# Kernel optimization log

Measured on AMD Instinct MI355X. Metric: run time of the kernel, lower is better.

Reference implementation:

```python
import jax, jax.numpy as jnp
import numpy as np

B, S, D, E, K = 4, 2048, 768, 8, 2


def setup_inputs() -> dict:
    key = jax.random.key(0)
    ks = jax.random.split(key, 5)
    s = 0.02
    return {
        "x": jax.random.normal(ks[0], (B, S, D), dtype=jnp.float32),
        "gate_w": jax.random.normal(ks[1], (D, E), dtype=jnp.float32) * s,
        "gate_b": jnp.zeros((E,), dtype=jnp.float32),
        "w1": jax.random.normal(ks[2], (E, D, D), dtype=jnp.float32) * s,
        "b1": jnp.zeros((E, D), dtype=jnp.float32),
        "w2": jax.random.normal(ks[3], (E, D, D), dtype=jnp.float32) * s,
        "b2": jnp.zeros((E, D), dtype=jnp.float32),
    }


def reference(x, gate_w, gate_b, w1, b1, w2, b2):
    # MoE forward, eval mode (no gate noise, dropout = identity)
    b, s, d = x.shape
    xf = x.reshape(-1, d)                                  # [T, D]
    T = xf.shape[0]

    gate_logits = xf @ gate_w + gate_b                     # [T, E]
    gate_scores = jax.nn.softmax(gate_logits, axis=-1)

    topv, topi = jax.lax.top_k(gate_scores, K)             # [T, K]
    topv = topv / (jnp.sum(topv, axis=-1, keepdims=True) + 1e-8)

    # scatter top-k weights into dense per-expert combine weights [T, E]
    comb = jnp.zeros((T, E), dtype=xf.dtype).at[
        jnp.arange(T)[:, None], topi].add(topv)

    # expert MLPs (dense over experts; combine weights zero-out unselected)
    h = jax.nn.relu(jnp.einsum('td,edh->teh', xf, w1) + b1)  # [T, E, D]
    y = jnp.einsum('teh,eho->teo', h, w2) + b2               # [T, E, D]
    out = jnp.einsum('te,teo->to', comb, y).reshape(b, s, -1)

    # load-balance aux loss (CV^2 of expert importance)
    importance = gate_scores.sum(axis=0)                   # [E]
    cv2 = importance.var() / (importance.mean() ** 2 + 1e-8)
    aux_loss = 0.01 * cv2
    return out, aux_loss
```

## Files before the change

kernel.cpp:

```cpp
#include <hip/hip_runtime.h>


#define T_TOK 8192
#define D_DIM 768
#define E_EXP 8
#define TK    16384

typedef __attribute__((ext_vector_type(4))) float f32x4;
typedef __attribute__((ext_vector_type(8))) short s16x8;
typedef __attribute__((ext_vector_type(8))) unsigned short u16x8;

static __device__ __forceinline__ unsigned short f2bf(float f) {
    union { float f; unsigned u; } v; v.f = f;
    unsigned r = v.u + 0x7FFFu + ((v.u >> 16) & 1u);
    return (unsigned short)(r >> 16);
}
static __device__ __forceinline__ float bf2f(unsigned short h) {
    union { unsigned u; float f; } v; v.u = ((unsigned)h) << 16;
    return v.f;
}

__global__ __launch_bounds__(256) void gate_kernel(
    const float* __restrict__ x, const float* __restrict__ gw,
    const float* __restrict__ gb, unsigned short* __restrict__ xb,
    int* __restrict__ ea, int* __restrict__ eb,
    float* __restrict__ wa, float* __restrict__ wb,
    int* __restrict__ counts, float* __restrict__ importance)
{
    __shared__ float s_imp[4][8];
    __shared__ int   s_cnt[4][8];
    const int tid = threadIdx.x, wid = tid >> 6, lane = tid & 63;
    const int wg = blockIdx.x * 4 + wid;

    float imp[8]; int cnt[8];
    #pragma unroll
    for (int e = 0; e < 8; ++e) { imp[e] = 0.f; cnt[e] = 0; }

    for (int i = 0; i < 8; ++i) {
        const int t = wg + i * 1024;
        const float* xr = x + (size_t)t * D_DIM;
        float xv[12];
        float acc[8];
        #pragma unroll
        for (int e = 0; e < 8; ++e) acc[e] = 0.f;
        #pragma unroll
        for (int j = 0; j < 12; ++j) {
            const int d = lane + j * 64;
            float v = xr[d];
            xv[j] = v;
            xb[(size_t)t * D_DIM + d] = f2bf(v);
        }
        #pragma unroll
        for (int j = 0; j < 12; ++j) {
            const int d = lane + j * 64;
            const f32x4* g = (const f32x4*)(gw + (size_t)d * 8);
            f32x4 g0 = g[0], g1 = g[1];
            float v = xv[j];
            acc[0] += v * g0[0]; acc[1] += v * g0[1];
            acc[2] += v * g0[2]; acc[3] += v * g0[3];
            acc[4] += v * g1[0]; acc[5] += v * g1[1];
            acc[6] += v * g1[2]; acc[7] += v * g1[3];
        }
        #pragma unroll
        for (int s = 1; s < 64; s <<= 1) {
            #pragma unroll
            for (int e = 0; e < 8; ++e) acc[e] += __shfl_xor(acc[e], s);
        }
        float lg[8], mx = -1e30f;
        #pragma unroll
        for (int e = 0; e < 8; ++e) { lg[e] = acc[e] + gb[e]; mx = fmaxf(mx, lg[e]); }
        float p[8], ssum = 0.f;
        #pragma unroll
        for (int e = 0; e < 8; ++e) { p[e] = expf(lg[e] - mx); ssum += p[e]; }
        float sc[8];
        float inv_s = 1.f / ssum;
        #pragma unroll
        for (int e = 0; e < 8; ++e) { sc[e] = p[e] * inv_s; imp[e] += sc[e]; }
        int i0 = 0;
        #pragma unroll
        for (int e = 1; e < 8; ++e) if (sc[e] > sc[i0]) i0 = e;
        int i1 = (i0 == 0) ? 1 : 0;
        #pragma unroll
        for (int e = 0; e < 8; ++e) if (e != i0 && sc[e] > sc[i1]) i1 = e;
        float v0 = sc[i0], v1 = sc[i1];
        float inv = 1.f / (v0 + v1 + 1e-8f);
        if (lane == 0) {
            ea[t] = i0; eb[t] = i1; wa[t] = v0 * inv; wb[t] = v1 * inv;
            cnt[i0]++; cnt[i1]++;
        }
    }
    if (lane == 0) {
        #pragma unroll
        for (int e = 0; e < 8; ++e) { s_imp[wid][e] = imp[e]; s_cnt[wid][e] = cnt[e]; }
    }
    __syncthreads();
    if (tid < 8) {
        float si = 0.f; int sc2 = 0;
        #pragma unroll
        for (int w = 0; w < 4; ++w) { si += s_imp[w][tid]; sc2 += s_cnt[w][tid]; }
        atomicAdd(importance + tid, si);
        atomicAdd(counts + tid, sc2);
    }
}

__global__ void prefix_aux_kernel(const int* __restrict__ counts, int* __restrict__ basep,
                                  int* __restrict__ cursor,
                                  const float* __restrict__ importance,
                                  float* __restrict__ aux_out)
{
    if (threadIdx.x == 0 && blockIdx.x == 0) {
        int b = 0;
        for (int e = 0; e < 8; ++e) { basep[e] = b; cursor[e] = b; b += counts[e]; }
        float mean = 0.f;
        for (int e = 0; e < 8; ++e) mean += importance[e];
        mean *= 0.125f;
        float var = 0.f;
        for (int e = 0; e < 8; ++e) { float d = importance[e] - mean; var += d * d; }
        var *= 0.125f;
        aux_out[0] = 0.01f * var / (mean * mean + 1e-8f);
    }
}

__global__ __launch_bounds__(256) void scatter_kernel(
    const int* __restrict__ ea, const int* __restrict__ eb,
    const float* __restrict__ wa, const float* __restrict__ wb,
    int* __restrict__ cursor, int* __restrict__ list,
    float* __restrict__ wgt, int* __restrict__ slot)
{
    const int t = blockIdx.x * 256 + threadIdx.x;
    const int lane = threadIdx.x & 63;
    #pragma unroll
    for (int k = 0; k < 2; ++k) {
        const int e = k ? eb[t] : ea[t];
        const float w = k ? wb[t] : wa[t];
        int pos = 0;
        for (int ex = 0; ex < 8; ++ex) {
            unsigned long long m = __ballot(e == ex);
            if (e == ex) {
                int leader = __ffsll((unsigned long long)m) - 1;
                int n = __popcll(m);
                int p0 = 0;
                if (lane == leader) p0 = atomicAdd(cursor + ex, n);
                p0 = __shfl(p0, leader);
                pos = p0 + __popcll(m & ((1ull << lane) - 1ull));
            }
        }
        list[pos] = t; wgt[pos] = w; slot[t * 2 + k] = pos;
    }
}

__global__ __launch_bounds__(256) void tconv_kernel(
    const float* __restrict__ w1, const float* __restrict__ w2,
    unsigned short* __restrict__ w1t, unsigned short* __restrict__ w2t)
{
    const int z = blockIdx.z;
    const float* src = (z < 8 ? w1 : w2) + (size_t)(z & 7) * D_DIM * D_DIM;
    unsigned short* dst = (z < 8 ? w1t : w2t) + (size_t)(z & 7) * D_DIM * D_DIM;
    __shared__ float tile[32][33];
    const int tx = threadIdx.x, ty = threadIdx.y;
    const int k0 = blockIdx.x * 32, n0 = blockIdx.y * 32;
    #pragma unroll
    for (int j = 0; j < 4; ++j)
        tile[ty + j * 8][tx] = src[(size_t)(k0 + ty + j * 8) * D_DIM + n0 + tx];
    __syncthreads();
    #pragma unroll
    for (int j = 0; j < 4; ++j)
        dst[(size_t)(n0 + ty + j * 8) * D_DIM + k0 + tx] = f2bf(tile[tx][ty + j * 8]);
}

template<int GATHER, int RELU>
__global__ __launch_bounds__(256) void moe_gemm_kernel(
    const unsigned short* __restrict__ A, const unsigned short* __restrict__ Bt,
    const float* __restrict__ bias, unsigned short* __restrict__ C,
    const int* __restrict__ counts, const int* __restrict__ basep,
    const int* __restrict__ list)
{
    const int e = blockIdx.z;
    const int count = counts[e];
    const int m0 = blockIdx.x * 128;
    if (m0 >= count) return;
    const int n0 = blockIdx.y * 128;
    const int base = basep[e];

    __shared__ unsigned short Al[128][40];
    __shared__ unsigned short Bl[128][40];

    const int tid = threadIdx.x;
    const int lane = tid & 63, wid = tid >> 6;
    const int wr = wid >> 1, wc = wid & 1;

    const int srow = tid >> 2;
    const int scol = (tid & 3) * 8;

    long ga0, ga1;
    {
        int r0 = m0 + srow;      r0 = r0 < count ? r0 : count - 1;
        int r1 = m0 + 64 + srow; r1 = r1 < count ? r1 : count - 1;
        long gr0, gr1;
        if (GATHER) { gr0 = list[base + r0]; gr1 = list[base + r1]; }
        else        { gr0 = base + r0;       gr1 = base + r1; }
        ga0 = gr0 * D_DIM; ga1 = gr1 * D_DIM;
    }
    const long gb0 = ((long)e * D_DIM + n0 + srow) * D_DIM;
    const long gb1 = ((long)e * D_DIM + n0 + 64 + srow) * D_DIM;

    f32x4 acc[4][4];
    #pragma unroll
    for (int mi = 0; mi < 4; ++mi)
        #pragma unroll
        for (int ni = 0; ni < 4; ++ni)
            acc[mi][ni] = (f32x4)(0.f);

    for (int k0 = 0; k0 < D_DIM; k0 += 32) {
        u16x8 a0  = *(const u16x8*)(A  + ga0 + k0 + scol);
        u16x8 a1  = *(const u16x8*)(A  + ga1 + k0 + scol);
        u16x8 b0  = *(const u16x8*)(Bt + gb0 + k0 + scol);
        u16x8 b1v = *(const u16x8*)(Bt + gb1 + k0 + scol);
        __syncthreads();
        *(u16x8*)&Al[srow][scol]      = a0;
        *(u16x8*)&Al[64 + srow][scol] = a1;
        *(u16x8*)&Bl[srow][scol]      = b0;
        *(u16x8*)&Bl[64 + srow][scol] = b1v;
        __syncthreads();

        s16x8 af[4], bf[4];
        #pragma unroll
        for (int mi = 0; mi < 4; ++mi)
            af[mi] = *(const s16x8*)&Al[wr * 64 + mi * 16 + (lane & 15)][(lane >> 4) * 8];
        #pragma unroll
        for (int ni = 0; ni < 4; ++ni)
            bf[ni] = *(const s16x8*)&Bl[wc * 64 + ni * 16 + (lane & 15)][(lane >> 4) * 8];
        #pragma unroll
        for (int mi = 0; mi < 4; ++mi)
            #pragma unroll
            for (int ni = 0; ni < 4; ++ni)
                acc[mi][ni] = __builtin_amdgcn_mfma_f32_16x16x32_bf16(
                    af[mi], bf[ni], acc[mi][ni], 0, 0, 0);
    }

    #pragma unroll
    for (int ni = 0; ni < 4; ++ni) {
        const int cn = n0 + wc * 64 + ni * 16 + (lane & 15);
        const float bv = bias[e * D_DIM + cn];
        #pragma unroll
        for (int mi = 0; mi < 4; ++mi) {
            #pragma unroll
            for (int j = 0; j < 4; ++j) {
                const int rm = m0 + wr * 64 + mi * 16 + (lane >> 4) * 4 + j;
                if (rm < count) {
                    float v = acc[mi][ni][j] + bv;
                    if (RELU) v = fmaxf(v, 0.f);
                    C[(size_t)(base + rm) * D_DIM + cn] = f2bf(v);
                }
            }
        }
    }
}

__global__ __launch_bounds__(256) void combine_kernel(
    const unsigned short* __restrict__ y, const int* __restrict__ slot,
    const float* __restrict__ wgt, float* __restrict__ out)
{
    const int g = blockIdx.x * 256 + threadIdx.x;
    const int t = g / 96;
    const int n = (g % 96) * 8;
    const int s0 = slot[t * 2], s1 = slot[t * 2 + 1];
    const float w0 = wgt[s0], w1 = wgt[s1];
    u16x8 ya = *(const u16x8*)(y + (size_t)s0 * D_DIM + n);
    u16x8 yb = *(const u16x8*)(y + (size_t)s1 * D_DIM + n);
    f32x4 o0, o1;
    #pragma unroll
    for (int i = 0; i < 4; ++i) o0[i] = w0 * bf2f(ya[i])     + w1 * bf2f(yb[i]);
    #pragma unroll
    for (int i = 0; i < 4; ++i) o1[i] = w0 * bf2f(ya[4 + i]) + w1 * bf2f(yb[4 + i]);
    float* op = out + (size_t)t * D_DIM + n;
    *(f32x4*)op       = o0;
    *(f32x4*)(op + 4) = o1;
}

extern "C" void kernel_launch(void* const* d_in, const int* in_sizes, int n_in,
                              void* d_out, int out_size, void* d_ws, size_t ws_size,
                              hipStream_t stream)
{
    const float* x  = (const float*)d_in[0];
    const float* gw = (const float*)d_in[1];
    const float* gb = (const float*)d_in[2];
    const float* w1 = (const float*)d_in[3];
    const float* b1 = (const float*)d_in[4];
    const float* w2 = (const float*)d_in[5];
    const float* b2 = (const float*)d_in[6];
    float* out = (float*)d_out;

    char* ws = (char*)d_ws;
    size_t off = 0;
    auto alloc = [&](size_t bytes) {
        char* p = ws + off; off += (bytes + 255) & ~(size_t)255; return p;
    };
    unsigned short* xb  = (unsigned short*)alloc((size_t)T_TOK * D_DIM * 2);
    unsigned short* w1t = (unsigned short*)alloc((size_t)E_EXP * D_DIM * D_DIM * 2);
    unsigned short* w2t = (unsigned short*)alloc((size_t)E_EXP * D_DIM * D_DIM * 2);
    unsigned short* h   = (unsigned short*)alloc((size_t)TK * D_DIM * 2);
    unsigned short* y   = (unsigned short*)alloc((size_t)TK * D_DIM * 2);
    int*   list = (int*)alloc(TK * 4);
    float* wgt  = (float*)alloc(TK * 4);
    int*   slot = (int*)alloc(TK * 4);
    int*   ea   = (int*)alloc(T_TOK * 4);
    int*   eb   = (int*)alloc(T_TOK * 4);
    float* wa   = (float*)alloc(T_TOK * 4);
    float* wb   = (float*)alloc(T_TOK * 4);
    int*   meta = (int*)alloc(256);
    int*   counts = meta;
    int*   basep  = meta + 8;
    int*   cursor = meta + 16;
    float* importance = (float*)(meta + 24);

    hipMemsetAsync(meta, 0, 256, stream);
    tconv_kernel<<<dim3(24, 24, 16), dim3(32, 8), 0, stream>>>(w1, w2, w1t, w2t);
    gate_kernel<<<256, 256, 0, stream>>>(x, gw, gb, xb, ea, eb, wa, wb, counts, importance);
    prefix_aux_kernel<<<1, 64, 0, stream>>>(counts, basep, cursor, importance,
                                            out + (out_size - 1));
    scatter_kernel<<<32, 256, 0, stream>>>(ea, eb, wa, wb, cursor, list, wgt, slot);
    moe_gemm_kernel<1, 1><<<dim3(64, 6, 8), 256, 0, stream>>>(xb, w1t, b1, h, counts, basep, list);
    moe_gemm_kernel<0, 0><<<dim3(64, 6, 8), 256, 0, stream>>>(h, w2t, b2, y, counts, basep, list);
    combine_kernel<<<3072, 256, 0, stream>>>(y, slot, wgt, out);
}
```

Measured before the change: 338.1 us.

## Load GEMM tiles directly to LDS and fold prefix/aux into gate kernel

The expert GEMM now uses global_load_lds to move A and B tiles from global memory straight into shared memory, skipping the register round trip. The LDS tiles switch to an unpadded 32-element row stride that this instruction needs. Separately, the prefix-sum and aux-loss kernel is merged into the gate kernel through a last-block-done atomic counter, which removes one launch. Dropping the padding can cause LDS bank conflicts on the fragment reads, and loads are still not double-buffered.

```diff
diff --git a/kernel.cpp b/kernel.cpp
--- a/kernel.cpp
+++ b/kernel.cpp
@@ -18,6 +18,13 @@
 static __device__ __forceinline__ float bf2f(unsigned short h) {
     union { unsigned u; float f; } v; v.u = ((unsigned)h) << 16;
     return v.f;
+}
+
+static __device__ __forceinline__ void gload_lds16(const unsigned short* g, unsigned short* l) {
+    __builtin_amdgcn_global_load_lds(
+        (const __attribute__((address_space(1))) unsigned int*)(const void*)g,
+        (__attribute__((address_space(3))) unsigned int*)(void*)l,
+        16, 0, 0);
 }
 
 __global__ __launch_bounds__(256) void gate_kernel(
@@ -25,7 +32,9 @@
     const float* __restrict__ gb, unsigned short* __restrict__ xb,
     int* __restrict__ ea, int* __restrict__ eb,
     float* __restrict__ wa, float* __restrict__ wb,
-    int* __restrict__ counts, float* __restrict__ importance)
+    int* __restrict__ counts, float* __restrict__ importance,
+    int* __restrict__ basep, int* __restrict__ cursor,
+    int* __restrict__ done, float* __restrict__ aux_out)
 {
     __shared__ float s_imp[4][8];
     __shared__ int   s_cnt[4][8];
@@ -101,23 +110,29 @@
         atomicAdd(importance + tid, si);
         atomicAdd(counts + tid, sc2);
     }
-}
-
-__global__ void prefix_aux_kernel(const int* __restrict__ counts, int* __restrict__ basep,
-                                  int* __restrict__ cursor,
-                                  const float* __restrict__ importance,
-                                  float* __restrict__ aux_out)
-{
-    if (threadIdx.x == 0 && blockIdx.x == 0) {
-        int b = 0;
-        for (int e = 0; e < 8; ++e) { basep[e] = b; cursor[e] = b; b += counts[e]; }
-        float mean = 0.f;
-        for (int e = 0; e < 8; ++e) mean += importance[e];
-        mean *= 0.125f;
-        float var = 0.f;
-        for (int e = 0; e < 8; ++e) { float d = importance[e] - mean; var += d * d; }
-        var *= 0.125f;
-        aux_out[0] = 0.01f * var / (mean * mean + 1e-8f);
+    __threadfence();
+    __syncthreads();
+    if (tid == 0) {
+        if (atomicAdd(done, 1) == (int)gridDim.x - 1) {
+            int c[8]; float im[8];
+            #pragma unroll
+            for (int e = 0; e < 8; ++e) {
+                c[e]  = atomicAdd(counts + e, 0);
+                im[e] = atomicAdd(importance + e, 0.0f);
+            }
+            int b = 0;
+            #pragma unroll
+            for (int e = 0; e < 8; ++e) { basep[e] = b; cursor[e] = b; b += c[e]; }
+            float mean = 0.f;
+            #pragma unroll
+            for (int e = 0; e < 8; ++e) mean += im[e];
+            mean *= 0.125f;
+            float var = 0.f;
+            #pragma unroll
+            for (int e = 0; e < 8; ++e) { float d = im[e] - mean; var += d * d; }
+            var *= 0.125f;
+            aux_out[0] = 0.01f * var / (mean * mean + 1e-8f);
+        }
     }
 }
 
@@ -182,27 +197,28 @@
     const int n0 = blockIdx.y * 128;
     const int base = basep[e];
 
-    __shared__ unsigned short Al[128][40];
-    __shared__ unsigned short Bl[128][40];
+    __shared__ unsigned short Al[128 * 32];
+    __shared__ unsigned short Bl[128 * 32];
 
     const int tid = threadIdx.x;
     const int lane = tid & 63, wid = tid >> 6;
     const int wr = wid >> 1, wc = wid & 1;
 
-    const int srow = tid >> 2;
-    const int scol = (tid & 3) * 8;
-
-    long ga0, ga1;
-    {
-        int r0 = m0 + srow;      r0 = r0 < count ? r0 : count - 1;
-        int r1 = m0 + 64 + srow; r1 = r1 < count ? r1 : count - 1;
-        long gr0, gr1;
-        if (GATHER) { gr0 = list[base + r0]; gr1 = list[base + r1]; }
-        else        { gr0 = base + r0;       gr1 = base + r1; }
-        ga0 = gr0 * D_DIM; ga1 = gr1 * D_DIM;
-    }
-    const long gb0 = ((long)e * D_DIM + n0 + srow) * D_DIM;
-    const long gb1 = ((long)e * D_DIM + n0 + 64 + srow) * D_DIM;
+    const int sr = wid * 16 + (lane >> 2);
+    const int sc = (lane & 3) * 8;
+
+    int r0 = m0 + sr;      if (r0 >= count) r0 = count - 1;
+    int r1 = m0 + 64 + sr; if (r1 >= count) r1 = count - 1;
+    const size_t t0 = GATHER ? (size_t)list[base + r0] : (size_t)(base + r0);
+    const size_t t1 = GATHER ? (size_t)list[base + r1] : (size_t)(base + r1);
+    const unsigned short* gA0 = A + t0 * D_DIM + sc;
+    const unsigned short* gA1 = A + t1 * D_DIM + sc;
+    const unsigned short* gB0 = Bt + ((size_t)e * D_DIM + n0 + sr) * D_DIM + sc;
+    const unsigned short* gB1 = Bt + ((size_t)e * D_DIM + n0 + 64 + sr) * D_DIM + sc;
+    unsigned short* lA0 = &Al[(wid * 16) * 32];
+    unsigned short* lA1 = &Al[(64 + wid * 16) * 32];
+    unsigned short* lB0 = &Bl[(wid * 16) * 32];
+    unsigned short* lB1 = &Bl[(64 + wid * 16) * 32];
 
     f32x4 acc[4][4];
     #pragma unroll
@@ -212,24 +228,20 @@
             acc[mi][ni] = (f32x4)(0.f);
 
     for (int k0 = 0; k0 < D_DIM; k0 += 32) {
-        u16x8 a0  = *(const u16x8*)(A  + ga0 + k0 + scol);
-        u16x8 a1  = *(const u16x8*)(A  + ga1 + k0 + scol);
-        u16x8 b0  = *(const u16x8*)(Bt + gb0 + k0 + scol);
-        u16x8 b1v = *(const u16x8*)(Bt + gb1 + k0 + scol);
         __syncthreads();
-        *(u16x8*)&Al[srow][scol]      = a0;
-        *(u16x8*)&Al[64 + srow][scol] = a1;
-        *(u16x8*)&Bl[srow][scol]      = b0;
-        *(u16x8*)&Bl[64 + srow][scol] = b1v;
+        gload_lds16(gA0 + k0, lA0);
+        gload_lds16(gA1 + k0, lA1);
+        gload_lds16(gB0 + k0, lB0);
+        gload_lds16(gB1 + k0, lB1);
         __syncthreads();
 
         s16x8 af[4], bf[4];
         #pragma unroll
         for (int mi = 0; mi < 4; ++mi)
-            af[mi] = *(const s16x8*)&Al[wr * 64 + mi * 16 + (lane & 15)][(lane >> 4) * 8];
+            af[mi] = *(const s16x8*)&Al[(wr * 64 + mi * 16 + (lane & 15)) * 32 + (lane >> 4) * 8];
         #pragma unroll
         for (int ni = 0; ni < 4; ++ni)
-            bf[ni] = *(const s16x8*)&Bl[wc * 64 + ni * 16 + (lane & 15)][(lane >> 4) * 8];
+            bf[ni] = *(const s16x8*)&Bl[(wc * 64 + ni * 16 + (lane & 15)) * 32 + (lane >> 4) * 8];
         #pragma unroll
         for (int mi = 0; mi < 4; ++mi)
             #pragma unroll
@@ -312,13 +324,13 @@
     int*   counts = meta;
     int*   basep  = meta + 8;
     int*   cursor = meta + 16;
-    float* importance = (float*)(meta + 24);
+    int*   done   = meta + 24;
+    float* importance = (float*)(meta + 32);
 
     hipMemsetAsync(meta, 0, 256, stream);
     tconv_kernel<<<dim3(24, 24, 16), dim3(32, 8), 0, stream>>>(w1, w2, w1t, w2t);
-    gate_kernel<<<256, 256, 0, stream>>>(x, gw, gb, xb, ea, eb, wa, wb, counts, importance);
-    prefix_aux_kernel<<<1, 64, 0, stream>>>(counts, basep, cursor, importance,
-                                            out + (out_size - 1));
+    gate_kernel<<<256, 256, 0, stream>>>(x, gw, gb, xb, ea, eb, wa, wb, counts, importance,
+                                         basep, cursor, done, out + (out_size - 1));
     scatter_kernel<<<32, 256, 0, stream>>>(ea, eb, wa, wb, cursor, list, wgt, slot);
     moe_gemm_kernel<1, 1><<<dim3(64, 6, 8), 256, 0, stream>>>(xb, w1t, b1, h, counts, basep, list);
     moe_gemm_kernel<0, 0><<<dim3(64, 6, 8), 256, 0, stream>>>(h, w2t, b2, y, counts, basep, list);
```

Measured after the change: 305.9 us. 1.11x faster.
